# Optimization experiments

Measured on AMD Instinct MI355X. Metric: run time of the kernel, lower is better.

Reference implementation:

```python
import jax, jax.numpy as jnp
import numpy as np

LN_EPS = 1e-5

def setup_inputs() -> dict:
    key = jax.random.key(0)
    ks = jax.random.split(key, 6)
    B, DETER, STOCH, ACT, HID = 131072, 256, 128, 16, 256
    deter = jax.random.normal(ks[0], (B, DETER), dtype=jnp.float32)
    stoch = jax.random.normal(ks[1], (B, STOCH), dtype=jnp.float32)
    action = jax.random.normal(ks[2], (B, ACT), dtype=jnp.float32)
    proj_w = jax.random.normal(ks[3], (STOCH + ACT, HID), dtype=jnp.float32) / np.sqrt(STOCH + ACT)
    proj_b = jnp.zeros((HID,), dtype=jnp.float32)
    core_w = jax.random.normal(ks[4], (HID + DETER, 3 * DETER), dtype=jnp.float32) / np.sqrt(HID + DETER)
    ln_g = jnp.ones((3 * DETER,), dtype=jnp.float32)
    ln_b = jnp.zeros((3 * DETER,), dtype=jnp.float32)
    return {"deter": deter, "stoch": stoch, "action": action,
            "proj_w": proj_w, "proj_b": proj_b, "core_w": core_w,
            "ln_g": ln_g, "ln_b": ln_b}

def _layernorm(x, g, b):
    mu = jnp.mean(x, axis=-1, keepdims=True)
    var = jnp.mean(jnp.square(x - mu), axis=-1, keepdims=True)
    return (x - mu) * jax.lax.rsqrt(var + LN_EPS) * g + b

def reference(deter, stoch, action, proj_w, proj_b, core_w, ln_g, ln_b):
    # stoch_action_proj: single Linear (mlp with no hidden layers)
    tokens = jnp.concatenate([stoch, action], axis=-1) @ proj_w + proj_b  # [B, hidden]
    parts = _layernorm(jnp.concatenate([tokens, deter], axis=-1) @ core_w, ln_g, ln_b)  # [B, 3*deter]
    d = parts.shape[-1] // 3
    reset, cand, update = parts[..., :d], parts[..., d:2 * d], parts[..., 2 * d:]
    reset = jax.nn.sigmoid(reset)
    cand = jnp.tanh(reset * cand)
    update = jax.nn.sigmoid(update - 1.0)
    return update * cand + (1.0 - update) * deter
```

## Files before the change

### kernel.cpp

```cpp
#include <hip/hip_runtime.h>


typedef _Float16 f16x8 __attribute__((ext_vector_type(8)));
typedef _Float16 f16x4 __attribute__((ext_vector_type(4)));
typedef float    f32x4 __attribute__((ext_vector_type(4)));

#define MFMA16(a, b, c) __builtin_amdgcn_mfma_f32_16x16x32_f16((a), (b), (c), 0, 0, 0)

#define LO_SCALE 2048.0f
#define LO_INV   (1.0f / 2048.0f)

__device__ __forceinline__ float sigmoid_f(float x) {
  return 1.0f / (1.0f + __expf(-x));
}
__device__ __forceinline__ float tanh_f(float x) {
  float ax = fabsf(x);
  float t = 1.0f - 2.0f / (__expf(2.0f * ax) + 1.0f);
  return copysignf(t, x);
}

__launch_bounds__(512, 4)
__global__ void minigru_fused(const float* __restrict__ deter,
                              const float* __restrict__ stoch,
                              const float* __restrict__ action,
                              const float* __restrict__ proj_w,
                              const float* __restrict__ proj_b,
                              const float* __restrict__ core_w,
                              const float* __restrict__ ln_g,
                              const float* __restrict__ ln_b,
                              float* __restrict__ out) {
  __shared__ char sm[65536];
  const int tid = threadIdx.x;
  const int lane = tid & 63;
  const int w = tid >> 6;
  const int l15 = lane & 15;
  const int grp = lane >> 4;
  const long row0 = (long)blockIdx.x * 32;

  auto addrH = [&](int row, int kbyte) -> char* {
    return sm + (row << 10) + (kbyte ^ ((row & 7) << 4));
  };
  auto addrL = [&](int row, int kbyte) -> char* {
    return sm + 32768 + (row << 10) + (kbyte ^ ((row & 7) << 4));
  };

  auto stage4 = [&](int r, int kbyte, float4 v) {
    f16x4 h, l;
    _Float16 h0 = (_Float16)v.x; h[0] = h0; l[0] = (_Float16)((v.x - (float)h0) * LO_SCALE);
    _Float16 h1 = (_Float16)v.y; h[1] = h1; l[1] = (_Float16)((v.y - (float)h1) * LO_SCALE);
    _Float16 h2 = (_Float16)v.z; h[2] = h2; l[2] = (_Float16)((v.z - (float)h2) * LO_SCALE);
    _Float16 h3 = (_Float16)v.w; h[3] = h3; l[3] = (_Float16)((v.w - (float)h3) * LO_SCALE);
    *(f16x4*)addrH(r, kbyte) = h;
    *(f16x4*)addrL(r, kbyte) = l;
  };

#pragma unroll
  for (int it = 0; it < 2; ++it) {
    int idx = it * 512 + tid;
    int r = idx >> 5, c4 = idx & 31;
    stage4(r, 512 + (c4 << 3), ((const float4*)stoch)[(size_t)(row0 + r) * 32 + c4]);
  }
  if (tid < 128) {
    int r = tid >> 2, c4 = tid & 3;
    stage4(r, 768 + (c4 << 3), ((const float4*)action)[(size_t)(row0 + r) * 4 + c4]);
    f16x4 z;
#pragma unroll
    for (int q = 0; q < 4; ++q) z[q] = (_Float16)0.0f;
    *(f16x4*)addrH(r, 800 + (c4 << 3)) = z;
    *(f16x4*)addrL(r, 800 + (c4 << 3)) = z;
  }
  __syncthreads();

  f32x4 accT[2][2];
#pragma unroll
  for (int rt = 0; rt < 2; ++rt)
#pragma unroll
    for (int ci = 0; ci < 2; ++ci)
#pragma unroll
      for (int q = 0; q < 4; ++q) accT[rt][ci][q] = 0.0f;

  for (int kb = 0; kb < 5; ++kb) {
    f16x8 ah[2], al[2];
#pragma unroll
    for (int rt = 0; rt < 2; ++rt) {
      int row = rt * 16 + l15;
      int kbyte = 512 + kb * 64 + grp * 16;
      ah[rt] = *(const f16x8*)addrH(row, kbyte);
      al[rt] = *(const f16x8*)addrL(row, kbyte);
    }
#pragma unroll
    for (int ci = 0; ci < 2; ++ci) {
      int ct = 2 * w + ci;
      f16x8 bh, bl;
#pragma unroll
      for (int j = 0; j < 8; ++j) {
        int k = kb * 32 + grp * 8 + j;
        float v = (k < 144) ? proj_w[k * 256 + ct * 16 + l15] : 0.0f;
        _Float16 hh = (_Float16)v;
        bh[j] = hh;
        bl[j] = (_Float16)((v - (float)hh) * LO_SCALE);
      }
      f32x4 tmp[2];
#pragma unroll
      for (int rt = 0; rt < 2; ++rt)
#pragma unroll
        for (int q = 0; q < 4; ++q) tmp[rt][q] = 0.0f;
#pragma unroll
      for (int rt = 0; rt < 2; ++rt) {
        accT[rt][ci] = MFMA16(ah[rt], bh, accT[rt][ci]);
        tmp[rt] = MFMA16(al[rt], bh, tmp[rt]);
        tmp[rt] = MFMA16(ah[rt], bl, tmp[rt]);
      }
#pragma unroll
      for (int rt = 0; rt < 2; ++rt)
#pragma unroll
        for (int q = 0; q < 4; ++q) accT[rt][ci][q] += tmp[rt][q] * LO_INV;
    }
  }

#pragma unroll
  for (int ci = 0; ci < 2; ++ci) {
    int colb = (2 * w + ci) * 16 + l15;
    float pb = proj_b[colb];
#pragma unroll
    for (int rt = 0; rt < 2; ++rt)
#pragma unroll
      for (int j = 0; j < 4; ++j) {
        int row = rt * 16 + grp * 4 + j;
        float tv = accT[rt][ci][j] + pb;
        _Float16 hh = (_Float16)tv;
        *(_Float16*)addrH(row, 2 * colb) = hh;
        *(_Float16*)addrL(row, 2 * colb) = (_Float16)((tv - (float)hh) * LO_SCALE);
      }
  }
  __syncthreads();

#pragma unroll
  for (int it = 0; it < 4; ++it) {
    int idx = it * 512 + tid;
    int r = idx >> 6, c4 = idx & 63;
    stage4(r, 512 + (c4 << 3), ((const float4*)deter)[(size_t)(row0 + r) * 64 + c4]);
  }
  __syncthreads();

  f32x4 acc[2][6];
#pragma unroll
  for (int rt = 0; rt < 2; ++rt)
#pragma unroll
    for (int ci = 0; ci < 6; ++ci)
#pragma unroll
      for (int q = 0; q < 4; ++q) acc[rt][ci][q] = 0.0f;

  int ctg[6];
#pragma unroll
  for (int ci = 0; ci < 6; ++ci) ctg[ci] = (ci >> 1) * 16 + 2 * w + (ci & 1);

  {
    float bc[8];
#pragma unroll
    for (int j = 0; j < 8; ++j)
      bc[j] = core_w[(grp * 8 + j) * 768 + ctg[0] * 16 + l15];

    for (int kb = 0; kb < 16; ++kb) {
      f16x8 ah[2], al[2];
#pragma unroll
      for (int rt = 0; rt < 2; ++rt) {
        int row = rt * 16 + l15;
        int kbyte = kb * 64 + grp * 16;
        ah[rt] = *(const f16x8*)addrH(row, kbyte);
        al[rt] = *(const f16x8*)addrL(row, kbyte);
      }
#pragma unroll
      for (int ci = 0; ci < 6; ++ci) {
        int kb2 = (ci == 5) ? kb + 1 : kb;
        int ci2 = (ci == 5) ? 0 : ci + 1;
        int kbc = (kb2 < 16) ? kb2 : 15;
        float bn[8];
        int nbase = (kbc * 32 + grp * 8) * 768 + ctg[ci2] * 16 + l15;
#pragma unroll
        for (int j = 0; j < 8; ++j) bn[j] = core_w[nbase + j * 768];

        f16x8 bh, bl;
#pragma unroll
        for (int j = 0; j < 8; ++j) {
          _Float16 hh = (_Float16)bc[j];
          bh[j] = hh;
          bl[j] = (_Float16)((bc[j] - (float)hh) * LO_SCALE);
        }
        f32x4 tmp[2];
#pragma unroll
        for (int rt = 0; rt < 2; ++rt)
#pragma unroll
          for (int q = 0; q < 4; ++q) tmp[rt][q] = 0.0f;
#pragma unroll
        for (int rt = 0; rt < 2; ++rt) {
          acc[rt][ci] = MFMA16(ah[rt], bh, acc[rt][ci]);
          tmp[rt] = MFMA16(al[rt], bh, tmp[rt]);
          tmp[rt] = MFMA16(ah[rt], bl, tmp[rt]);
        }
#pragma unroll
        for (int rt = 0; rt < 2; ++rt)
#pragma unroll
          for (int q = 0; q < 4; ++q) acc[rt][ci][q] += tmp[rt][q] * LO_INV;
#pragma unroll
        for (int j = 0; j < 8; ++j) bc[j] = bn[j];
      }
    }
  }
  __syncthreads();

  float2* red2 = (float2*)sm;
  float2* ln2 = ((float2*)sm) + 256;

  float s[2][4], q[2][4];
#pragma unroll
  for (int rt = 0; rt < 2; ++rt)
#pragma unroll
    for (int j = 0; j < 4; ++j) {
      float ss = 0.0f, qq = 0.0f;
#pragma unroll
      for (int ci = 0; ci < 6; ++ci) {
        float v = acc[rt][ci][j];
        ss += v;
        qq += v * v;
      }
      s[rt][j] = ss;
      q[rt][j] = qq;
    }
#pragma unroll
  for (int off = 1; off < 16; off <<= 1) {
#pragma unroll
    for (int rt = 0; rt < 2; ++rt)
#pragma unroll
      for (int j = 0; j < 4; ++j) {
        s[rt][j] += __shfl_xor(s[rt][j], off);
        q[rt][j] += __shfl_xor(q[rt][j], off);
      }
  }
#pragma unroll
  for (int j = 0; j < 4; ++j) {
    if (l15 == j) {
#pragma unroll
      for (int rt = 0; rt < 2; ++rt) {
        float2 p;
        p.x = s[rt][j];
        p.y = q[rt][j];
        red2[w * 32 + rt * 16 + grp * 4 + j] = p;
      }
    }
  }
  __syncthreads();
  if (tid < 32) {
    float ssum = 0.0f, qsum = 0.0f;
#pragma unroll
    for (int ww = 0; ww < 8; ++ww) {
      float2 p = red2[ww * 32 + tid];
      ssum += p.x;
      qsum += p.y;
    }
    float mu = ssum * (1.0f / 768.0f);
    float var = qsum * (1.0f / 768.0f) - mu * mu;
    float2 o;
    o.x = mu;
    o.y = rsqrtf(var + 1e-5f);
    ln2[tid] = o;
  }
  __syncthreads();

  float gv[6], bv[6];
#pragma unroll
  for (int ci = 0; ci < 6; ++ci) {
    int col = ctg[ci] * 16 + l15;
    gv[ci] = ln_g[col];
    bv[ci] = ln_b[col];
  }
#pragma unroll
  for (int rt = 0; rt < 2; ++rt) {
#pragma unroll
    for (int j = 0; j < 4; ++j) {
      int rowl = rt * 16 + grp * 4 + j;
      float2 mr = ln2[rowl];
      float vals[6];
#pragma unroll
      for (int ci = 0; ci < 6; ++ci)
        vals[ci] = (acc[rt][ci][j] - mr.x) * mr.y * gv[ci] + bv[ci];
#pragma unroll
      for (int p = 0; p < 2; ++p) {
        float rr = sigmoid_f(vals[p]);
        float cc = tanh_f(rr * vals[2 + p]);
        float uu = sigmoid_f(vals[4 + p] - 1.0f);
        int gcol = (2 * w + p) * 16 + l15;
        size_t o = (size_t)(row0 + rowl) * 256 + gcol;
        float dt = deter[o];
        out[o] = uu * cc + (1.0f - uu) * dt;
      }
    }
  }
}

extern "C" void kernel_launch(void* const* d_in, const int* in_sizes, int n_in,
                              void* d_out, int out_size, void* d_ws, size_t ws_size,
                              hipStream_t stream) {
  const float* deter  = (const float*)d_in[0];
  const float* stoch  = (const float*)d_in[1];
  const float* action = (const float*)d_in[2];
  const float* proj_w = (const float*)d_in[3];
  const float* proj_b = (const float*)d_in[4];
  const float* core_w = (const float*)d_in[5];
  const float* ln_g   = (const float*)d_in[6];
  const float* ln_b   = (const float*)d_in[7];
  float* out = (float*)d_out;

  (void)in_sizes; (void)n_in; (void)out_size; (void)d_ws; (void)ws_size;

  minigru_fused<<<dim3(4096), 512, 0, stream>>>(deter, stoch, action,
                                                proj_w, proj_b, core_w,
                                                ln_g, ln_b, out);
}
```

Baseline: 1.283 ms.

## Drop split-fp16 compensation and prepack fp16 weights into the workspace

Removes the hi/lo fp16 split emulation of fp32 matmuls, so each tile runs one MFMA instead of three and LDS staging is halved. Two small prep kernels convert core_w and proj_w once per call into fp16 fragments laid out for the MFMA operands, so the main kernel loads them as single vectors. The smaller shared buffer allows launch bounds of 8 blocks per CU. The cost is lower matmul precision (plain fp16 inputs with fp32 accumulation), which risks exceeding the accuracy tolerance. The prepacked path runs only when the workspace is large enough.

```diff
diff --git a/kernel.cpp b/kernel.cpp
--- a/kernel.cpp
+++ b/kernel.cpp
@@ -7,8 +7,34 @@
 
 #define MFMA16(a, b, c) __builtin_amdgcn_mfma_f32_16x16x32_f16((a), (b), (c), 0, 0, 0)
 
-#define LO_SCALE 2048.0f
-#define LO_INV   (1.0f / 2048.0f)
+#define PF_OFF 393216
+#define WS_NEEDED ((size_t)868352)
+
+__global__ void prep_core(const float* __restrict__ cw, _Float16* __restrict__ ws) {
+  int t = blockIdx.x * 256 + threadIdx.x;
+  int l15 = t & 15, grp = (t >> 4) & 3, ctk = t >> 6;
+  int ct = ctk % 48, kb = ctk / 48;
+  int n = ct * 16 + l15;
+  f16x8 h;
+#pragma unroll
+  for (int j = 0; j < 8; ++j)
+    h[j] = (_Float16)cw[(kb * 32 + grp * 8 + j) * 768 + n];
+  ((f16x8*)ws)[t] = h;
+}
+
+__global__ void prep_proj(const float* __restrict__ pw, _Float16* __restrict__ ws) {
+  int t = blockIdx.x * 256 + threadIdx.x;
+  int l15 = t & 15, grp = (t >> 4) & 3, ctk = t >> 6;
+  int ct = ctk & 15, kb = ctk >> 4;
+  int n = ct * 16 + l15;
+  f16x8 h;
+#pragma unroll
+  for (int j = 0; j < 8; ++j) {
+    int k = kb * 32 + grp * 8 + j;
+    h[j] = (_Float16)((k < 144) ? pw[k * 256 + n] : 0.0f);
+  }
+  ((f16x8*)(ws + PF_OFF))[t] = h;
+}
 
 __device__ __forceinline__ float sigmoid_f(float x) {
   return 1.0f / (1.0f + __expf(-x));
@@ -19,17 +45,19 @@
   return copysignf(t, x);
 }
 
-__launch_bounds__(512, 4)
-__global__ void minigru_fused(const float* __restrict__ deter,
-                              const float* __restrict__ stoch,
-                              const float* __restrict__ action,
-                              const float* __restrict__ proj_w,
-                              const float* __restrict__ proj_b,
-                              const float* __restrict__ core_w,
-                              const float* __restrict__ ln_g,
-                              const float* __restrict__ ln_b,
-                              float* __restrict__ out) {
-  __shared__ char sm[65536];
+template <bool PREPPED>
+__launch_bounds__(512, 8)
+__global__ void minigru_main(const float* __restrict__ deter,
+                             const float* __restrict__ stoch,
+                             const float* __restrict__ action,
+                             const float* __restrict__ proj_w,
+                             const float* __restrict__ proj_b,
+                             const float* __restrict__ core_w,
+                             const float* __restrict__ ln_g,
+                             const float* __restrict__ ln_b,
+                             const _Float16* __restrict__ wf,
+                             float* __restrict__ out) {
+  __shared__ char sm[32768];
   const int tid = threadIdx.x;
   const int lane = tid & 63;
   const int w = tid >> 6;
@@ -37,21 +65,16 @@
   const int grp = lane >> 4;
   const long row0 = (long)blockIdx.x * 32;
 
-  auto addrH = [&](int row, int kbyte) -> char* {
+  auto addrX = [&](int row, int kbyte) -> char* {
     return sm + (row << 10) + (kbyte ^ ((row & 7) << 4));
   };
-  auto addrL = [&](int row, int kbyte) -> char* {
-    return sm + 32768 + (row << 10) + (kbyte ^ ((row & 7) << 4));
-  };
-
   auto stage4 = [&](int r, int kbyte, float4 v) {
-    f16x4 h, l;
-    _Float16 h0 = (_Float16)v.x; h[0] = h0; l[0] = (_Float16)((v.x - (float)h0) * LO_SCALE);
-    _Float16 h1 = (_Float16)v.y; h[1] = h1; l[1] = (_Float16)((v.y - (float)h1) * LO_SCALE);
-    _Float16 h2 = (_Float16)v.z; h[2] = h2; l[2] = (_Float16)((v.z - (float)h2) * LO_SCALE);
-    _Float16 h3 = (_Float16)v.w; h[3] = h3; l[3] = (_Float16)((v.w - (float)h3) * LO_SCALE);
-    *(f16x4*)addrH(r, kbyte) = h;
-    *(f16x4*)addrL(r, kbyte) = l;
+    f16x4 h;
+    h[0] = (_Float16)v.x;
+    h[1] = (_Float16)v.y;
+    h[2] = (_Float16)v.z;
+    h[3] = (_Float16)v.w;
+    *(f16x4*)addrX(r, kbyte) = h;
   };
 
 #pragma unroll
@@ -66,8 +89,7 @@
     f16x4 z;
 #pragma unroll
     for (int q = 0; q < 4; ++q) z[q] = (_Float16)0.0f;
-    *(f16x4*)addrH(r, 800 + (c4 << 3)) = z;
-    *(f16x4*)addrL(r, 800 + (c4 << 3)) = z;
+    *(f16x4*)addrX(r, 800 + (c4 << 3)) = z;
   }
   __syncthreads();
 
@@ -80,41 +102,26 @@
       for (int q = 0; q < 4; ++q) accT[rt][ci][q] = 0.0f;
 
   for (int kb = 0; kb < 5; ++kb) {
-    f16x8 ah[2], al[2];
-#pragma unroll
-    for (int rt = 0; rt < 2; ++rt) {
-      int row = rt * 16 + l15;
-      int kbyte = 512 + kb * 64 + grp * 16;
-      ah[rt] = *(const f16x8*)addrH(row, kbyte);
-      al[rt] = *(const f16x8*)addrL(row, kbyte);
-    }
+    f16x8 ah[2];
+#pragma unroll
+    for (int rt = 0; rt < 2; ++rt)
+      ah[rt] = *(const f16x8*)addrX(rt * 16 + l15, 512 + kb * 64 + grp * 16);
 #pragma unroll
     for (int ci = 0; ci < 2; ++ci) {
       int ct = 2 * w + ci;
-      f16x8 bh, bl;
-#pragma unroll
-      for (int j = 0; j < 8; ++j) {
-        int k = kb * 32 + grp * 8 + j;
-        float v = (k < 144) ? proj_w[k * 256 + ct * 16 + l15] : 0.0f;
-        _Float16 hh = (_Float16)v;
-        bh[j] = hh;
-        bl[j] = (_Float16)((v - (float)hh) * LO_SCALE);
-      }
-      f32x4 tmp[2];
+      f16x8 bh;
+      if constexpr (PREPPED) {
+        bh = ((const f16x8*)(wf + PF_OFF))[(kb * 16 + ct) * 64 + lane];
+      } else {
+#pragma unroll
+        for (int j = 0; j < 8; ++j) {
+          int k = kb * 32 + grp * 8 + j;
+          bh[j] = (_Float16)((k < 144) ? proj_w[k * 256 + ct * 16 + l15] : 0.0f);
+        }
+      }
 #pragma unroll
       for (int rt = 0; rt < 2; ++rt)
-#pragma unroll
-        for (int q = 0; q < 4; ++q) tmp[rt][q] = 0.0f;
-#pragma unroll
-      for (int rt = 0; rt < 2; ++rt) {
         accT[rt][ci] = MFMA16(ah[rt], bh, accT[rt][ci]);
-        tmp[rt] = MFMA16(al[rt], bh, tmp[rt]);
-        tmp[rt] = MFMA16(ah[rt], bl, tmp[rt]);
-      }
-#pragma unroll
-      for (int rt = 0; rt < 2; ++rt)
-#pragma unroll
-        for (int q = 0; q < 4; ++q) accT[rt][ci][q] += tmp[rt][q] * LO_INV;
     }
   }
 
@@ -127,10 +134,7 @@
 #pragma unroll
       for (int j = 0; j < 4; ++j) {
         int row = rt * 16 + grp * 4 + j;
-        float tv = accT[rt][ci][j] + pb;
-        _Float16 hh = (_Float16)tv;
-        *(_Float16*)addrH(row, 2 * colb) = hh;
-        *(_Float16*)addrL(row, 2 * colb) = (_Float16)((tv - (float)hh) * LO_SCALE);
+        *(_Float16*)addrX(row, 2 * colb) = (_Float16)(accT[rt][ci][j] + pb);
       }
   }
   __syncthreads();
@@ -155,56 +159,25 @@
 #pragma unroll
   for (int ci = 0; ci < 6; ++ci) ctg[ci] = (ci >> 1) * 16 + 2 * w + (ci & 1);
 
-  {
-    float bc[8];
-#pragma unroll
-    for (int j = 0; j < 8; ++j)
-      bc[j] = core_w[(grp * 8 + j) * 768 + ctg[0] * 16 + l15];
-
-    for (int kb = 0; kb < 16; ++kb) {
-      f16x8 ah[2], al[2];
-#pragma unroll
-      for (int rt = 0; rt < 2; ++rt) {
-        int row = rt * 16 + l15;
-        int kbyte = kb * 64 + grp * 16;
-        ah[rt] = *(const f16x8*)addrH(row, kbyte);
-        al[rt] = *(const f16x8*)addrL(row, kbyte);
-      }
-#pragma unroll
-      for (int ci = 0; ci < 6; ++ci) {
-        int kb2 = (ci == 5) ? kb + 1 : kb;
-        int ci2 = (ci == 5) ? 0 : ci + 1;
-        int kbc = (kb2 < 16) ? kb2 : 15;
-        float bn[8];
-        int nbase = (kbc * 32 + grp * 8) * 768 + ctg[ci2] * 16 + l15;
-#pragma unroll
-        for (int j = 0; j < 8; ++j) bn[j] = core_w[nbase + j * 768];
-
-        f16x8 bh, bl;
-#pragma unroll
-        for (int j = 0; j < 8; ++j) {
-          _Float16 hh = (_Float16)bc[j];
-          bh[j] = hh;
-          bl[j] = (_Float16)((bc[j] - (float)hh) * LO_SCALE);
-        }
-        f32x4 tmp[2];
-#pragma unroll
-        for (int rt = 0; rt < 2; ++rt)
-#pragma unroll
-          for (int q = 0; q < 4; ++q) tmp[rt][q] = 0.0f;
-#pragma unroll
-        for (int rt = 0; rt < 2; ++rt) {
-          acc[rt][ci] = MFMA16(ah[rt], bh, acc[rt][ci]);
-          tmp[rt] = MFMA16(al[rt], bh, tmp[rt]);
-          tmp[rt] = MFMA16(ah[rt], bl, tmp[rt]);
-        }
-#pragma unroll
-        for (int rt = 0; rt < 2; ++rt)
-#pragma unroll
-          for (int q = 0; q < 4; ++q) acc[rt][ci][q] += tmp[rt][q] * LO_INV;
-#pragma unroll
-        for (int j = 0; j < 8; ++j) bc[j] = bn[j];
-      }
+  for (int kb = 0; kb < 16; ++kb) {
+    f16x8 ah[2];
+#pragma unroll
+    for (int rt = 0; rt < 2; ++rt)
+      ah[rt] = *(const f16x8*)addrX(rt * 16 + l15, kb * 64 + grp * 16);
+#pragma unroll
+    for (int ci = 0; ci < 6; ++ci) {
+      f16x8 bh;
+      if constexpr (PREPPED) {
+        bh = ((const f16x8*)wf)[(kb * 48 + ctg[ci]) * 64 + lane];
+      } else {
+        int nbase = (kb * 32 + grp * 8) * 768 + ctg[ci] * 16 + l15;
+#pragma unroll
+        for (int j = 0; j < 8; ++j)
+          bh[j] = (_Float16)core_w[nbase + j * 768];
+      }
+#pragma unroll
+      for (int rt = 0; rt < 2; ++rt)
+        acc[rt][ci] = MFMA16(ah[rt], bh, acc[rt][ci]);
     }
   }
   __syncthreads();
@@ -212,9 +185,9 @@
   float2* red2 = (float2*)sm;
   float2* ln2 = ((float2*)sm) + 256;
 
-  float s[2][4], q[2][4];
-#pragma unroll
-  for (int rt = 0; rt < 2; ++rt)
+#pragma unroll
+  for (int rt = 0; rt < 2; ++rt) {
+    float s[4], q[4];
 #pragma unroll
     for (int j = 0; j < 4; ++j) {
       float ss = 0.0f, qq = 0.0f;
@@ -224,27 +197,23 @@
         ss += v;
         qq += v * v;
       }
-      s[rt][j] = ss;
-      q[rt][j] = qq;
-    }
-#pragma unroll
-  for (int off = 1; off < 16; off <<= 1) {
-#pragma unroll
-    for (int rt = 0; rt < 2; ++rt)
+      s[j] = ss;
+      q[j] = qq;
+    }
+#pragma unroll
+    for (int off = 1; off < 16; off <<= 1) {
 #pragma unroll
       for (int j = 0; j < 4; ++j) {
-        s[rt][j] += __shfl_xor(s[rt][j], off);
-        q[rt][j] += __shfl_xor(q[rt][j], off);
-      }
-  }
-#pragma unroll
-  for (int j = 0; j < 4; ++j) {
-    if (l15 == j) {
-#pragma unroll
-      for (int rt = 0; rt < 2; ++rt) {
+        s[j] += __shfl_xor(s[j], off);
+        q[j] += __shfl_xor(q[j], off);
+      }
+    }
+#pragma unroll
+    for (int j = 0; j < 4; ++j) {
+      if (l15 == j) {
         float2 p;
-        p.x = s[rt][j];
-        p.y = q[rt][j];
+        p.x = s[j];
+        p.y = q[j];
         red2[w * 32 + rt * 16 + grp * 4 + j] = p;
       }
     }
@@ -309,11 +278,18 @@
   const float* core_w = (const float*)d_in[5];
   const float* ln_g   = (const float*)d_in[6];
   const float* ln_b   = (const float*)d_in[7];
+  _Float16* wf = (_Float16*)d_ws;
   float* out = (float*)d_out;
 
-  (void)in_sizes; (void)n_in; (void)out_size; (void)d_ws; (void)ws_size;
-
-  minigru_fused<<<dim3(4096), 512, 0, stream>>>(deter, stoch, action,
-                                                proj_w, proj_b, core_w,
-                                                ln_g, ln_b, out);
-}
+  (void)in_sizes; (void)n_in; (void)out_size;
+
+  if (ws_size >= WS_NEEDED) {
+    prep_core<<<dim3(192), 256, 0, stream>>>(core_w, wf);
+    prep_proj<<<dim3(20), 256, 0, stream>>>(proj_w, wf);
+    minigru_main<true><<<dim3(4096), 512, 0, stream>>>(
+        deter, stoch, action, proj_w, proj_b, core_w, ln_g, ln_b, wf, out);
+  } else {
+    minigru_main<false><<<dim3(4096), 512, 0, stream>>>(
+        deter, stoch, action, proj_w, proj_b, core_w, ln_g, ln_b, wf, out);
+  }
+}
```

New measurement: 1.201 ms. 1.07x faster.
